# Optimization experiments

Hardware: AMD Instinct MI355X
Metric: run time of the kernel (lower is better)

The kernel has to match this reference:

```python
import jax, jax.numpy as jnp
import numpy as np
from jax import lax

HEADS, DHEAD, LMARK, PINV_ITERS = 8, 64, 256, 6
LN_EPS = 1e-5
DIM_IN, DIM_HID, N_CLASSES, N_INST = 1024, 512, 2, 16384


def layer_norm(x, g, b):
    mu = x.mean(-1, keepdims=True)
    var = ((x - mu) ** 2).mean(-1, keepdims=True)
    return (x - mu) * lax.rsqrt(var + LN_EPS) * g + b


def pinv_iter(x):
    # Newton-Schulz Moore-Penrose iteration (lucidrains nystrom-attention)
    ax = jnp.abs(x)
    z = jnp.swapaxes(x, -1, -2) / (ax.sum(-1).max() * ax.sum(-2).max())
    I = jnp.eye(x.shape[-1], dtype=x.dtype)
    for _ in range(PINV_ITERS):
        xz = x @ z
        z = 0.25 * z @ (13.0 * I - xz @ (15.0 * I - xz @ (7.0 * I - xz)))
    return z


def nystrom_attention(x, qkv_w, out_w, out_b, res_w):
    b, n, _ = x.shape
    pad = (-n) % LMARK  # pad at FRONT so n divisible by num_landmarks
    xp = jnp.pad(x, ((0, 0), (pad, 0), (0, 0)))
    npad = n + pad
    qkv = xp @ qkv_w.T  # (b, npad, 3*h*d)
    q, k, v = jnp.split(qkv, 3, axis=-1)
    sh = lambda t: t.reshape(b, npad, HEADS, DHEAD).transpose(0, 2, 1, 3)  # bhnd
    q, k, v = sh(q), sh(k), sh(v)
    q = q * (DHEAD ** -0.5)
    l = npad // LMARK  # tokens per landmark
    lm = lambda t: t.reshape(b, HEADS, LMARK, l, DHEAD).mean(3)
    ql, kl = lm(q), lm(k)
    a1 = jax.nn.softmax(jnp.einsum('bhid,bhjd->bhij', q, kl), -1)   # (b,h,npad,m)
    a2 = jax.nn.softmax(jnp.einsum('bhid,bhjd->bhij', ql, kl), -1)  # (b,h,m,m)
    a3 = jax.nn.softmax(jnp.einsum('bhid,bhjd->bhij', ql, k), -1)   # (b,h,m,npad)
    out = (a1 @ pinv_iter(a2)) @ (a3 @ v)
    # depthwise residual conv over sequence dim per head: kernel (33,1)
    res = lax.conv_general_dilated(v, res_w, (1, 1), [(16, 16), (0, 0)],
                                   dimension_numbers=('NCHW', 'OIHW', 'NCHW'),
                                   feature_group_count=HEADS)
    out = out + res
    out = out.transpose(0, 2, 1, 3).reshape(b, npad, HEADS * DHEAD)
    out = out @ out_w.T + out_b
    return out[:, -n:]


def depthwise(x, w, b, k):
    y = lax.conv_general_dilated(x, w, (1, 1), [(k // 2, k // 2)] * 2,
                                 dimension_numbers=('NCHW', 'OIHW', 'NCHW'),
                                 feature_group_count=x.shape[1])
    return y + b[None, :, None, None]


def ppeg(x, w7, b7, w5, b5, w3, b3):
    B, n1, C = x.shape
    cls_t, feat = x[:, :1], x[:, 1:]
    H = int(round(float(np.sqrt(n1 - 1))))
    f = feat.transpose(0, 2, 1).reshape(B, C, H, H)
    f = f + depthwise(f, w7, b7, 7) + depthwise(f, w5, b5, 5) + depthwise(f, w3, b3, 3)
    f = f.reshape(B, C, H * H).transpose(0, 2, 1)
    return jnp.concatenate([cls_t, f], axis=1)


def setup_inputs() -> dict:
    key = jax.random.key(0)
    ks = jax.random.split(key, 32)
    s = 0.02
    inner = HEADS * DHEAD
    d = {
        'X': jax.random.normal(ks[0], (1, N_INST, DIM_IN), jnp.float32),
        'fc1_w': jax.random.normal(ks[1], (DIM_HID, DIM_IN)) * s,
        'fc1_b': jnp.zeros((DIM_HID,)),
        'cls_token': jax.random.normal(ks[2], (1, 1, DIM_HID)),
        'ln1_g': jnp.ones((DIM_HID,)), 'ln1_b': jnp.zeros((DIM_HID,)),
        'qkv1_w': jax.random.normal(ks[3], (3 * inner, DIM_HID)) * s,
        'out1_w': jax.random.normal(ks[4], (DIM_HID, inner)) * s,
        'out1_b': jnp.zeros((DIM_HID,)),
        'res1_w': jax.random.normal(ks[5], (HEADS, 1, 33, 1)) * s,
        'w7': jax.random.normal(ks[6], (DIM_HID, 1, 7, 7)) * s, 'b7': jnp.zeros((DIM_HID,)),
        'w5': jax.random.normal(ks[7], (DIM_HID, 1, 5, 5)) * s, 'b5': jnp.zeros((DIM_HID,)),
        'w3': jax.random.normal(ks[8], (DIM_HID, 1, 3, 3)) * s, 'b3': jnp.zeros((DIM_HID,)),
        'ln2_g': jnp.ones((DIM_HID,)), 'ln2_b': jnp.zeros((DIM_HID,)),
        'qkv2_w': jax.random.normal(ks[9], (3 * inner, DIM_HID)) * s,
        'out2_w': jax.random.normal(ks[10], (DIM_HID, inner)) * s,
        'out2_b': jnp.zeros((DIM_HID,)),
        'res2_w': jax.random.normal(ks[11], (HEADS, 1, 33, 1)) * s,
        'lnf_g': jnp.ones((DIM_HID,)), 'lnf_b': jnp.zeros((DIM_HID,)),
        'fc2_w': jax.random.normal(ks[12], (N_CLASSES, DIM_HID)) * s,
        'fc2_b': jnp.zeros((N_CLASSES,)),
    }
    return d


def reference(X, fc1_w, fc1_b, cls_token, ln1_g, ln1_b, qkv1_w, out1_w, out1_b, res1_w,
              w7, b7, w5, b5, w3, b3, ln2_g, ln2_b, qkv2_w, out2_w, out2_b, res2_w,
              lnf_g, lnf_b, fc2_w, fc2_b):
    h = jax.nn.relu(X @ fc1_w.T + fc1_b)  # (1, N, dim_hid)
    B, Hn, C = h.shape
    _H = int(np.ceil(np.sqrt(Hn)))
    add_len = _H * _H - Hn
    h = jnp.concatenate([h, h[:, :add_len]], axis=1)  # pad to square by cycling
    h = jnp.concatenate([jnp.broadcast_to(cls_token, (B, 1, C)), h], axis=1)
    h = h + nystrom_attention(layer_norm(h, ln1_g, ln1_b), qkv1_w, out1_w, out1_b, res1_w)
    h = ppeg(h, w7, b7, w5, b5, w3, b3)
    h = h + nystrom_attention(layer_norm(h, ln2_g, ln2_b), qkv2_w, out2_w, out2_b, res2_w)
    h = layer_norm(h, lnf_g, lnf_b)[:, 0]
    return h @ fc2_w.T + fc2_b  # (1, n_classes)
```

## Files before the change

kernel.cpp:

```cpp
#include <hip/hip_runtime.h>
#include <hip/hip_bf16.h>

static const int S    = 16640;
static const int PADR = 255;
static const int NT   = 16385;
static const int CH   = 512;

typedef unsigned short u16;
typedef __attribute__((ext_vector_type(8))) short short8_t;
typedef __attribute__((ext_vector_type(4))) float float4_t;

__device__ __forceinline__ float b2f(u16 x) {
  union { unsigned u; float f; } t; t.u = (unsigned)x << 16; return t.f;
}
__device__ __forceinline__ u16 f2b(float x) {
  union { float f; unsigned u; } t; t.f = x;
  unsigned r = t.u + 0x7fff + ((t.u >> 16) & 1);
  return (u16)(r >> 16);
}

__device__ __forceinline__ void gload_lds16(const u16* g, u16* l) {
  __builtin_amdgcn_global_load_lds(
      (const __attribute__((address_space(1))) unsigned int*)(g),
      (__attribute__((address_space(3))) unsigned int*)(l), 16, 0, 0);
}

__device__ __forceinline__ float warpSum(float v) {
#pragma unroll
  for (int off = 32; off; off >>= 1) v += __shfl_xor(v, off);
  return v;
}
__device__ __forceinline__ float warpMax(float v) {
#pragma unroll
  for (int off = 32; off; off >>= 1) v = fmaxf(v, __shfl_xor(v, off));
  return v;
}
__device__ __forceinline__ float blockSum(float v) {
  __shared__ float sm[8];
  int lane = threadIdx.x & 63, wv = threadIdx.x >> 6;
  v = warpSum(v);
  __syncthreads();
  if (lane == 0) sm[wv] = v;
  __syncthreads();
  float t = 0.f;
  int nw = blockDim.x >> 6;
  for (int i = 0; i < nw; i++) t += sm[i];
  return t;
}
__device__ __forceinline__ float blockMax(float v) {
  __shared__ float sm[8];
  int lane = threadIdx.x & 63, wv = threadIdx.x >> 6;
  v = warpMax(v);
  __syncthreads();
  if (lane == 0) sm[wv] = v;
  __syncthreads();
  float t = -1e30f;
  int nw = blockDim.x >> 6;
  for (int i = 0; i < nw; i++) t = fmaxf(t, sm[i]);
  return t;
}

__global__ __launch_bounds__(256) void cvt_f2b(const float* __restrict__ in,
                                               u16* __restrict__ out, long n) {
  long i = ((long)blockIdx.x * 256 + threadIdx.x) * 4;
  if (i + 3 < n) {
    float4 v = *(const float4*)(in + i);
    out[i] = f2b(v.x); out[i + 1] = f2b(v.y); out[i + 2] = f2b(v.z); out[i + 3] = f2b(v.w);
  } else {
    for (long j = i; j < n; j++) out[j] = f2b(in[j]);
  }
}

__global__ __launch_bounds__(256) void wm_transpose(const float* __restrict__ Wm,
                                                    u16* __restrict__ WmT) {
  int n = blockIdx.x, head = blockIdx.y, k = threadIdx.x;
  WmT[((long)head * 64 + n) * 256 + k] = f2b(Wm[(long)head * 16384 + k * 64 + n]);
}

__global__ __launch_bounds__(256) void mfma_gemm_qkv(
    const u16* __restrict__ A, const u16* __restrict__ B, float alpha,
    u16* __restrict__ q_o, u16* __restrict__ k_o, u16* __restrict__ v_o, long s64)
{
  __shared__ u16 As[128 * 32];
  __shared__ u16 Bs[128 * 32];
  const int tid = threadIdx.x;
  const int nwg = gridDim.x * gridDim.y;
  int lid = blockIdx.y * gridDim.x + blockIdx.x;
  {
    const int qq = nwg >> 3, rr = nwg & 7;
    const int xcd = lid & 7, loc = lid >> 3;
    lid = (xcd < rr ? xcd * (qq + 1) : rr * (qq + 1) + (xcd - rr) * qq) + loc;
  }
  const int m0 = (lid / gridDim.x) * 128, n0 = (lid % gridDim.x) * 128;
  const int wid = tid >> 6, lane = tid & 63;
  const int wr = wid >> 1, wc = wid & 1;
  const int l15 = lane & 15, l16 = lane >> 4;
  const int r_loc = lane >> 2;
  const int cseg  = lane & 3;
  float4_t acc[4][4] = {};

  for (int k0 = 0; k0 < 512; k0 += 32) {
#pragma unroll
    for (int inst = 0; inst < 2; inst++) {
      const int rbase = wid * 32 + inst * 16;
      const int r = rbase + r_loc;
      const int gseg = cseg ^ ((r >> 1) & 3);
      gload_lds16(A + (long)(m0 + r) * 512 + k0 + gseg * 8, &As[rbase * 32]);
      gload_lds16(B + (long)(n0 + r) * 512 + k0 + gseg * 8, &Bs[rbase * 32]);
    }
    __syncthreads();
    short8_t af[4], bfr[4];
#pragma unroll
    for (int i = 0; i < 4; i++) {
      int row = wr * 64 + i * 16 + l15;
      af[i] = *(const short8_t*)&As[row * 32 + (l16 ^ ((row >> 1) & 3)) * 8];
      int rowb = wc * 64 + i * 16 + l15;
      bfr[i] = *(const short8_t*)&Bs[rowb * 32 + (l16 ^ ((rowb >> 1) & 3)) * 8];
    }
#pragma unroll
    for (int i = 0; i < 4; i++)
#pragma unroll
      for (int j = 0; j < 4; j++)
        acc[i][j] = __builtin_amdgcn_mfma_f32_16x16x32_bf16(af[i], bfr[j], acc[i][j], 0, 0, 0);
    __syncthreads();
  }

#pragma unroll
  for (int mi = 0; mi < 4; mi++) {
#pragma unroll
    for (int ni = 0; ni < 4; ni++) {
#pragma unroll
      for (int j = 0; j < 4; j++) {
        int r = m0 + wr * 64 + mi * 16 + (l16 << 2) + j;
        int c = n0 + wc * 64 + ni * 16 + l15;
        int sec = c >> 9, hcol = c & 511;
        int head = hcol >> 6, d = hcol & 63;
        u16* dst = (sec == 0) ? q_o : (sec == 1 ? k_o : v_o);
        float o = (sec == 0) ? acc[mi][ni][j] * alpha : acc[mi][ni][j];
        dst[(long)head * s64 + (long)r * 64 + d] = f2b(o);
      }
    }
  }
}

template <typename TA, int EPI>
__global__ __launch_bounds__(256) void mfma_gemm(
    const TA* __restrict__ A, const u16* __restrict__ B, float* __restrict__ C,
    const float* __restrict__ bias, int M, int N, int K,
    int lda, int ldb, int ldc,
    float alpha, float beta,
    u16* __restrict__ q_o, u16* __restrict__ k_o, u16* __restrict__ v_o, long s64)
{
  __shared__ u16 As[128][36];
  __shared__ u16 Bs[128][36];
  const int tid = threadIdx.x;
  const int nwg = gridDim.x * gridDim.y;
  int lid = blockIdx.y * gridDim.x + blockIdx.x;
  {
    const int qq = nwg >> 3, rr = nwg & 7;
    const int xcd = lid & 7, loc = lid >> 3;
    lid = (xcd < rr ? xcd * (qq + 1) : rr * (qq + 1) + (xcd - rr) * qq) + loc;
  }
  const int m0 = (lid / gridDim.x) * 128, n0 = (lid % gridDim.x) * 128;
  const int wid = tid >> 6, lane = tid & 63;
  const int wr = wid >> 1, wc = wid & 1;
  const int l15 = lane & 15, l16 = lane >> 4;
  const int arow = tid >> 1, aseg = (tid & 1) * 16;
  float4_t acc[4][4] = {};

  for (int k0 = 0; k0 < K; k0 += 32) {
    {
      int gm = m0 + arow;
      u16 tmp[16];
      if (gm < M) {
        const TA* src = A + (long)gm * lda + k0 + aseg;
        if constexpr (sizeof(TA) == 2) {
          *(short8_t*)&tmp[0] = *(const short8_t*)src;
          *(short8_t*)&tmp[8] = *(const short8_t*)(src + 8);
        } else {
#pragma unroll
          for (int i4 = 0; i4 < 4; i4++) {
            float4 f = *(const float4*)((const float*)src + i4 * 4);
            tmp[i4 * 4 + 0] = f2b(f.x); tmp[i4 * 4 + 1] = f2b(f.y);
            tmp[i4 * 4 + 2] = f2b(f.z); tmp[i4 * 4 + 3] = f2b(f.w);
          }
        }
      } else {
#pragma unroll
        for (int i = 0; i < 16; i++) tmp[i] = 0;
      }
      *(short8_t*)&As[arow][aseg]     = *(short8_t*)&tmp[0];
      *(short8_t*)&As[arow][aseg + 8] = *(short8_t*)&tmp[8];
    }
    {
      int gn = n0 + arow;
      short8_t v0 = {}, v1 = {};
      if (gn < N) {
        const u16* src = B + (long)gn * ldb + k0 + aseg;
        v0 = *(const short8_t*)src; v1 = *(const short8_t*)(src + 8);
      }
      *(short8_t*)&Bs[arow][aseg]     = v0;
      *(short8_t*)&Bs[arow][aseg + 8] = v1;
    }
    __syncthreads();
    short8_t af[4], bfr[4];
#pragma unroll
    for (int i = 0; i < 4; i++)
      af[i] = *(const short8_t*)&As[wr * 64 + i * 16 + l15][l16 * 8];
#pragma unroll
    for (int i = 0; i < 4; i++)
      bfr[i] = *(const short8_t*)&Bs[wc * 64 + i * 16 + l15][l16 * 8];
#pragma unroll
    for (int i = 0; i < 4; i++)
#pragma unroll
      for (int j = 0; j < 4; j++)
        acc[i][j] = __builtin_amdgcn_mfma_f32_16x16x32_bf16(af[i], bfr[j], acc[i][j], 0, 0, 0);
    __syncthreads();
  }

#pragma unroll
  for (int mi = 0; mi < 4; mi++) {
#pragma unroll
    for (int ni = 0; ni < 4; ni++) {
#pragma unroll
      for (int j = 0; j < 4; j++) {
        int r = m0 + wr * 64 + mi * 16 + l16 * 4 + j;
        int c = n0 + wc * 64 + ni * 16 + l15;
        if (r >= M || c >= N) continue;
        float v = acc[mi][ni][j];
        if constexpr (EPI == 0) {
          long idx = (long)r * ldc + c;
          float o = alpha * v;
          if (bias) o += bias[c];
          if (beta != 0.f) o += beta * C[idx];
          C[idx] = o;
        } else if constexpr (EPI == 1) {
          long idx = (long)r * ldc + c;
          C[idx] = fmaxf(v + bias[c], 0.f);
        } else {
          int sec = c >> 9, hcol = c & 511;
          int head = hcol >> 6, d = hcol & 63;
          u16* dst = (sec == 0) ? q_o : (sec == 1 ? k_o : v_o);
          float o = (sec == 0) ? v * alpha : v;
          dst[(long)head * s64 + (long)r * 64 + d] = f2b(o);
        }
      }
    }
  }
}

template <int MODE, int PREC>
__global__ __launch_bounds__(256) void pinv_gemm(
    const float* __restrict__ A, const float* __restrict__ B,
    float* __restrict__ C, float* __restrict__ C2, float alpha, float beta)
{
  __shared__ u16 Ah[32][36], Bh[32][36];
  __shared__ u16 Al[PREC ? 32 : 1][36], Bl[PREC ? 32 : 1][36];
  const int tid = threadIdx.x;
  const long zoff = (long)blockIdx.z << 16;
  A += zoff; B += zoff; C += zoff;
  if constexpr (MODE == 3) C2 += zoff;
  const int m0 = blockIdx.y * 32, n0 = blockIdx.x * 32;
  const int wid = tid >> 6, lane = tid & 63;
  const int wr = wid >> 1, wc = wid & 1;
  const int l15 = lane & 15, l16 = lane >> 4;
  const int arow = tid >> 3, acol = (tid & 7) * 4;
  float4_t acc = {};

  for (int k0 = 0; k0 < 256; k0 += 32) {
    {
      float4 va = *(const float4*)(A + (long)(m0 + arow) * 256 + k0 + acol);
      float4 vb = *(const float4*)(B + (long)(k0 + arow) * 256 + n0 + acol);
      float fa[4] = {va.x, va.y, va.z, va.w};
      float fb[4] = {vb.x, vb.y, vb.z, vb.w};
#pragma unroll
      for (int i = 0; i < 4; i++) {
        u16 hi = f2b(fa[i]);
        Ah[arow][acol + i] = hi;
        u16 hj = f2b(fb[i]);
        Bh[acol + i][arow] = hj;
        if constexpr (PREC) {
          Al[arow][acol + i] = f2b(fa[i] - b2f(hi));
          Bl[acol + i][arow] = f2b(fb[i] - b2f(hj));
        }
      }
    }
    __syncthreads();
    short8_t ah = *(const short8_t*)&Ah[wr * 16 + l15][l16 * 8];
    short8_t bh = *(const short8_t*)&Bh[wc * 16 + l15][l16 * 8];
    acc = __builtin_amdgcn_mfma_f32_16x16x32_bf16(ah, bh, acc, 0, 0, 0);
    if constexpr (PREC) {
      short8_t al = *(const short8_t*)&Al[wr * 16 + l15][l16 * 8];
      short8_t bl = *(const short8_t*)&Bl[wc * 16 + l15][l16 * 8];
      acc = __builtin_amdgcn_mfma_f32_16x16x32_bf16(ah, bl, acc, 0, 0, 0);
      acc = __builtin_amdgcn_mfma_f32_16x16x32_bf16(al, bh, acc, 0, 0, 0);
    }
    __syncthreads();
  }

#pragma unroll
  for (int j = 0; j < 4; j++) {
    int r = m0 + wr * 16 + l16 * 4 + j;
    int c = n0 + wc * 16 + l15;
    long idx = (long)r * 256 + c;
    float v = acc[j];
    if constexpr (MODE == 0) {
      C[idx] = alpha * v;
    } else if constexpr (MODE == 3) {
      C[idx] = v;
      C2[idx] = ((r == c) ? beta : 0.f) - v;
    } else {
      C[idx] = ((r == c) ? beta : 0.f) - v;
    }
  }
}

__global__ __launch_bounds__(256) void a2_fused(
    const u16* __restrict__ qlb, const u16* __restrict__ klb,
    float* __restrict__ a2)
{
  __shared__ u16 KW[256 * 72];
  const int tid = threadIdx.x;
  const int w = tid >> 6, lane = tid & 63;
  const int l15 = lane & 15, l16 = lane >> 4;
  const int head = blockIdx.y;
  const int row0 = blockIdx.x * 64 + w * 16;

  const u16* klh = klb + (long)head * 16384;
#pragma unroll
  for (int i = 0; i < 4; i++) {
    int idx = tid + i * 256;
    int row = idx >> 2, seg = (idx & 3) << 4;
    const u16* src = klh + row * 64 + seg;
    *(short8_t*)&KW[row * 72 + seg]     = *(const short8_t*)src;
    *(short8_t*)&KW[row * 72 + seg + 8] = *(const short8_t*)(src + 8);
  }
  short8_t aq[2];
#pragma unroll
  for (int slab = 0; slab < 2; slab++)
    aq[slab] = *(const short8_t*)(qlb + (long)head * 16384 + (long)(row0 + l15) * 64 + slab * 32 + l16 * 8);
  __syncthreads();

  float4_t sacc[16] = {};
#pragma unroll
  for (int nt = 0; nt < 16; nt++)
#pragma unroll
    for (int slab = 0; slab < 2; slab++) {
      short8_t bfr = *(const short8_t*)&KW[(nt * 16 + l15) * 72 + slab * 32 + l16 * 8];
      sacc[nt] = __builtin_amdgcn_mfma_f32_16x16x32_bf16(aq[slab], bfr, sacc[nt], 0, 0, 0);
    }
#pragma unroll
  for (int reg = 0; reg < 4; reg++) {
    float m = -1e30f;
#pragma unroll
    for (int nt = 0; nt < 16; nt++) m = fmaxf(m, sacc[nt][reg]);
#pragma unroll
    for (int mk = 1; mk <= 8; mk <<= 1) m = fmaxf(m, __shfl_xor(m, mk));
    float s = 0.f;
#pragma unroll
    for (int nt = 0; nt < 16; nt++) { float e = __expf(sacc[nt][reg] - m); sacc[nt][reg] = e; s += e; }
#pragma unroll
    for (int mk = 1; mk <= 8; mk <<= 1) s += __shfl_xor(s, mk);
    float rcp = 1.f / s;
#pragma unroll
    for (int nt = 0; nt < 16; nt++)
      a2[(long)head * 65536 + (long)(row0 + 4 * l16 + reg) * 256 + nt * 16 + l15] =
          sacc[nt][reg] * rcp;
  }
}

__global__ __launch_bounds__(256) void attn_a1(
    const u16* __restrict__ qb, const u16* __restrict__ klb,
    const u16* __restrict__ WmT, float* __restrict__ F, long s64)
{
  __shared__ u16 KW[256 * 72];
  __shared__ u16 Ps[64 * 136];
  const int tid = threadIdx.x;
  const int w = tid >> 6, lane = tid & 63;
  const int l15 = lane & 15, l16 = lane >> 4;
  const int head = blockIdx.y;
  const int row0 = blockIdx.x * 64 + w * 16;

  const u16* klh = klb + (long)head * 16384;
#pragma unroll
  for (int i = 0; i < 4; i++) {
    int idx = tid + i * 256;
    int row = idx >> 2, seg = (idx & 3) << 4;
    const u16* src = klh + row * 64 + seg;
    *(short8_t*)&KW[row * 72 + seg]     = *(const short8_t*)src;
    *(short8_t*)&KW[row * 72 + seg + 8] = *(const short8_t*)(src + 8);
  }
  short8_t aq[2];
#pragma unroll
  for (int slab = 0; slab < 2; slab++)
    aq[slab] = *(const short8_t*)(qb + (long)head * s64 + (long)(row0 + l15) * 64 + slab * 32 + l16 * 8);
  __syncthreads();

  float4_t sacc[16] = {};
#pragma unroll
  for (int nt = 0; nt < 16; nt++)
#pragma unroll
    for (int slab = 0; slab < 2; slab++) {
      short8_t bfr = *(const short8_t*)&KW[(nt * 16 + l15) * 72 + slab * 32 + l16 * 8];
      sacc[nt] = __builtin_amdgcn_mfma_f32_16x16x32_bf16(aq[slab], bfr, sacc[nt], 0, 0, 0);
    }
  float rcp[4];
#pragma unroll
  for (int reg = 0; reg < 4; reg++) {
    float m = -1e30f;
#pragma unroll
    for (int nt = 0; nt < 16; nt++) m = fmaxf(m, sacc[nt][reg]);
#pragma unroll
    for (int mk = 1; mk <= 8; mk <<= 1) m = fmaxf(m, __shfl_xor(m, mk));
    float s = 0.f;
#pragma unroll
    for (int nt = 0; nt < 16; nt++) { float e = __expf(sacc[nt][reg] - m); sacc[nt][reg] = e; s += e; }
#pragma unroll
    for (int mk = 1; mk <= 8; mk <<= 1) s += __shfl_xor(s, mk);
    rcp[reg] = 1.f / s;
  }
  __syncthreads();

  const u16* wmh = WmT + (long)head * 16384;
#pragma unroll
  for (int i = 0; i < 4; i++) {
    int idx = tid + i * 256;
    int row = idx >> 4, seg = (idx & 15) << 4;
    const u16* src = wmh + row * 256 + seg;
    *(short8_t*)&KW[row * 264 + seg]     = *(const short8_t*)src;
    *(short8_t*)&KW[row * 264 + seg + 8] = *(const short8_t*)(src + 8);
  }
#pragma unroll
  for (int nt = 0; nt < 8; nt++)
#pragma unroll
    for (int reg = 0; reg < 4; reg++)
      Ps[(w * 16 + 4 * l16 + reg) * 136 + nt * 16 + l15] = f2b(sacc[nt][reg]);
  __syncthreads();

  float4_t oacc[4] = {};
#pragma unroll
  for (int ks = 0; ks < 4; ks++) {
    short8_t pa = *(const short8_t*)&Ps[(w * 16 + l15) * 136 + ks * 32 + l16 * 8];
#pragma unroll
    for (int vt = 0; vt < 4; vt++) {
      short8_t bv = *(const short8_t*)&KW[(vt * 16 + l15) * 264 + ks * 32 + l16 * 8];
      oacc[vt] = __builtin_amdgcn_mfma_f32_16x16x32_bf16(pa, bv, oacc[vt], 0, 0, 0);
    }
  }
#pragma unroll
  for (int nt = 8; nt < 16; nt++)
#pragma unroll
    for (int reg = 0; reg < 4; reg++)
      Ps[(w * 16 + 4 * l16 + reg) * 136 + (nt - 8) * 16 + l15] = f2b(sacc[nt][reg]);
#pragma unroll
  for (int ks = 4; ks < 8; ks++) {
    short8_t pa = *(const short8_t*)&Ps[(w * 16 + l15) * 136 + (ks - 4) * 32 + l16 * 8];
#pragma unroll
    for (int vt = 0; vt < 4; vt++) {
      short8_t bv = *(const short8_t*)&KW[(vt * 16 + l15) * 264 + ks * 32 + l16 * 8];
      oacc[vt] = __builtin_amdgcn_mfma_f32_16x16x32_bf16(pa, bv, oacc[vt], 0, 0, 0);
    }
  }
#pragma unroll
  for (int vt = 0; vt < 4; vt++)
#pragma unroll
    for (int reg = 0; reg < 4; reg++) {
      int r = row0 + 4 * l16 + reg;
      F[(long)r * CH + head * 64 + vt * 16 + l15] = oacc[vt][reg] * rcp[reg];
    }
}

__global__ __launch_bounds__(256) void attn_a3v_split(
    const u16* __restrict__ qlb, const u16* __restrict__ kb,
    const u16* __restrict__ vb,
    float* __restrict__ pm, float* __restrict__ pl, float* __restrict__ poacc,
    long s64)
{
  __shared__ u16 Vt[64][136];
  __shared__ u16 Kt[128 * 72];
  __shared__ u16 Ps[4][16][136];
  const int tid = threadIdx.x;
  const int w = tid >> 6, lane = tid & 63;
  const int l15 = lane & 15, l16 = lane >> 4;
  const int head = blockIdx.y;
  const int split = blockIdx.z;
  const int row0 = blockIdx.x * 64 + w * 16;

  short8_t aq[2];
#pragma unroll
  for (int slab = 0; slab < 2; slab++)
    aq[slab] = *(const short8_t*)(qlb + (long)head * 16384 + (long)(row0 + l15) * 64 + slab * 32 + l16 * 8);

  float m[4], l[4];
  float4_t oacc[4] = {};
#pragma unroll
  for (int r = 0; r < 4; r++) { m[r] = -1e30f; l[r] = 0.f; }

  const u16* kh = kb + (long)head * s64;
  const u16* vh = vb + (long)head * s64;
  const int vrow = tid >> 1, vhalf = (tid & 1) * 32;

  const int kt0 = split * 10;
  for (int kt = kt0; kt < kt0 + 10; kt++) {
    const int j0 = kt * 128;
    __syncthreads();
    {
      const u16* src = vh + (long)(j0 + vrow) * 64 + vhalf;
#pragma unroll
      for (int i = 0; i < 32; i++) Vt[vhalf + i][vrow] = src[i];
    }
#pragma unroll
    for (int i = 0; i < 2; i++) {
      int idx = tid + i * 256;
      int row = idx >> 2, seg = (idx & 3) << 4;
      const u16* src = kh + (long)(j0 + row) * 64 + seg;
      *(short8_t*)&Kt[row * 72 + seg]     = *(const short8_t*)src;
      *(short8_t*)&Kt[row * 72 + seg + 8] = *(const short8_t*)(src + 8);
    }
    __syncthreads();
    float4_t sacc[8] = {};
#pragma unroll
    for (int nt = 0; nt < 8; nt++)
#pragma unroll
      for (int slab = 0; slab < 2; slab++) {
        short8_t bfr = *(const short8_t*)&Kt[(nt * 16 + l15) * 72 + slab * 32 + l16 * 8];
        sacc[nt] = __builtin_amdgcn_mfma_f32_16x16x32_bf16(aq[slab], bfr, sacc[nt], 0, 0, 0);
      }
    float scale[4];
#pragma unroll
    for (int reg = 0; reg < 4; reg++) {
      float tm = -1e30f;
#pragma unroll
      for (int nt = 0; nt < 8; nt++) tm = fmaxf(tm, sacc[nt][reg]);
#pragma unroll
      for (int mk = 1; mk <= 8; mk <<= 1) tm = fmaxf(tm, __shfl_xor(tm, mk));
      float nm = fmaxf(m[reg], tm);
      scale[reg] = __expf(m[reg] - nm);
      m[reg] = nm;
      float ts = 0.f;
#pragma unroll
      for (int nt = 0; nt < 8; nt++) {
        float e = __expf(sacc[nt][reg] - nm);
        sacc[nt][reg] = e; ts += e;
      }
#pragma unroll
      for (int mk = 1; mk <= 8; mk <<= 1) ts += __shfl_xor(ts, mk);
      l[reg] = l[reg] * scale[reg] + ts;
#pragma unroll
      for (int vt = 0; vt < 4; vt++) oacc[vt][reg] *= scale[reg];
    }
#pragma unroll
    for (int nt = 0; nt < 8; nt++)
#pragma unroll
      for (int reg = 0; reg < 4; reg++)
        Ps[w][4 * l16 + reg][nt * 16 + l15] = f2b(sacc[nt][reg]);
#pragma unroll
    for (int ks = 0; ks < 4; ks++) {
      short8_t pa = *(const short8_t*)&Ps[w][l15][ks * 32 + l16 * 8];
#pragma unroll
      for (int vt = 0; vt < 4; vt++) {
        short8_t bv = *(const short8_t*)&Vt[vt * 16 + l15][ks * 32 + l16 * 8];
        oacc[vt] = __builtin_amdgcn_mfma_f32_16x16x32_bf16(pa, bv, oacc[vt], 0, 0, 0);
      }
    }
  }
#pragma unroll
  for (int reg = 0; reg < 4; reg++) {
    int r = row0 + 4 * l16 + reg;
    long pidx = ((long)(head * 13 + split) << 8) + r;
    if (l15 == 0) { pm[pidx] = m[reg]; pl[pidx] = l[reg]; }
#pragma unroll
    for (int vt = 0; vt < 4; vt++)
      poacc[(pidx << 6) + vt * 16 + l15] = oacc[vt][reg];
  }
}

__global__ __launch_bounds__(64) void a3v_merge(const float* __restrict__ pm,
    const float* __restrict__ pl, const float* __restrict__ poacc,
    float* __restrict__ w3v)
{
  int hb = blockIdx.x;
  int head = hb >> 8, row = hb & 255;
  int d = threadIdx.x;
  float M = -1e30f;
  for (int sp = 0; sp < 13; sp++)
    M = fmaxf(M, pm[((long)(head * 13 + sp) << 8) + row]);
  float num = 0.f, den = 0.f;
  for (int sp = 0; sp < 13; sp++) {
    long pidx = ((long)(head * 13 + sp) << 8) + row;
    float sc = __expf(pm[pidx] - M);
    den += pl[pidx] * sc;
    num += poacc[(pidx << 6) + d] * sc;
  }
  w3v[((long)head << 14) + ((long)row << 6) + d] = num / den;
}

template <bool BT, int MODE>
__global__ __launch_bounds__(256) void mm_kernel(
    const float* __restrict__ A, const float* __restrict__ Bm, float* __restrict__ C,
    const float* __restrict__ bias,
    int M, int N, int K, int lda, int ldb, int ldc,
    long sA, long sB, long sC, float alpha, float beta, long s64)
{
  __shared__ float As[16][64];
  __shared__ float Bs[16][64];
  const int bz = blockIdx.z;
  A  += (long)bz * sA;
  Bm += (long)bz * sB;
  C  += (long)bz * sC;
  const int m0 = blockIdx.y * 64, n0 = blockIdx.x * 64;
  const int tid = threadIdx.x;
  const int tm = tid >> 4, tn = tid & 15;
  const int ar = tid >> 2;
  const int ac = (tid & 3) << 2;
  float acc[4][4] = {};
  for (int k0 = 0; k0 < K; k0 += 16) {
#pragma unroll
    for (int i = 0; i < 4; i++) {
      int gm = m0 + ar, gk = k0 + ac + i;
      As[ac + i][ar] = (gm < M && gk < K) ? A[(long)gm * lda + gk] : 0.f;
    }
    if constexpr (BT) {
#pragma unroll
      for (int i = 0; i < 4; i++) {
        int gn = n0 + ar, gk = k0 + ac + i;
        Bs[ac + i][ar] = (gn < N && gk < K) ? Bm[(long)gn * ldb + gk] : 0.f;
      }
    } else {
      int bk = tid >> 4;
      int bn = (tid & 15) << 2;
#pragma unroll
      for (int i = 0; i < 4; i++) {
        int gk = k0 + bk, gn = n0 + bn + i;
        Bs[bk][bn + i] = (gk < K && gn < N) ? Bm[(long)gk * ldb + gn] : 0.f;
      }
    }
    __syncthreads();
#pragma unroll
    for (int kk = 0; kk < 16; kk++) {
      float a[4], b[4];
#pragma unroll
      for (int i = 0; i < 4; i++) { a[i] = As[kk][tm * 4 + i]; b[i] = Bs[kk][tn * 4 + i]; }
#pragma unroll
      for (int i = 0; i < 4; i++)
#pragma unroll
        for (int j = 0; j < 4; j++)
          acc[i][j] = fmaf(a[i], b[j], acc[i][j]);
    }
    __syncthreads();
  }
#pragma unroll
  for (int i = 0; i < 4; i++) {
    int row = m0 + tm * 4 + i;
    if (row >= M) continue;
#pragma unroll
    for (int j = 0; j < 4; j++) {
      int col = n0 + tn * 4 + j;
      if (col >= N) continue;
      long idx = (long)row * ldc + col;
      float v = acc[i][j];
      float o = alpha * v;
      if (bias) o += bias[col];
      C[idx] = (beta != 0.f) ? o + beta * C[idx] : o;
    }
  }
}

__global__ void cls_copy(const float* __restrict__ c, float* __restrict__ h) {
  h[threadIdx.x] = c[threadIdx.x];
}

__global__ __launch_bounds__(256) void ln_pad_b(const float* __restrict__ h,
    const float* __restrict__ g, const float* __restrict__ b,
    u16* __restrict__ out, int pad)
{
  int s = blockIdx.x, t = threadIdx.x;
  u16* o = out + (long)s * CH;
  if (s < pad) { o[t] = 0; o[t + 256] = 0; return; }
  const float* x = h + (long)(s - pad) * CH;
  float x0 = x[t], x1 = x[t + 256];
  float mu = blockSum(x0 + x1) * (1.f / 512.f);
  float d0 = x0 - mu, d1 = x1 - mu;
  float var = blockSum(d0 * d0 + d1 * d1) * (1.f / 512.f);
  float rs = rsqrtf(var + 1e-5f);
  o[t]       = f2b(d0 * rs * g[t]       + b[t]);
  o[t + 256] = f2b(d1 * rs * g[t + 256] + b[t + 256]);
}

__global__ __launch_bounds__(64) void landmark_b2(const u16* __restrict__ q,
    const u16* __restrict__ k,
    float* __restrict__ ql, float* __restrict__ kl,
    u16* __restrict__ qlb, u16* __restrict__ klb) {
  int isK = blockIdx.x >> 11;
  int hb = blockIdx.x & 2047;
  int d = threadIdx.x;
  int hh = hb >> 8, j = hb & 255;
  const u16* base = isK ? k : q;
  const u16* src = base + ((long)hh * S + (long)j * 65) * 64 + d;
  float s = 0.f;
  for (int g2 = 0; g2 < 65; g2++) s += b2f(src[(long)g2 * 64]);
  s *= (1.f / 65.f);
  float* outf = isK ? kl : ql;
  u16* outb = isK ? klb : qlb;
  outf[(long)hb * 64 + d] = s;
  outb[(long)hb * 64 + d] = f2b(s);
}

__global__ __launch_bounds__(256) void colabs(const float* __restrict__ a2, float* __restrict__ cs) {
  int hb = blockIdx.x; int hh = hb >> 8, j = hb & 255;
  float s = blockSum(fabsf(a2[((long)hh * 256 + threadIdx.x) * 256 + j]));
  if (threadIdx.x == 0) cs[hb] = s;
}
__global__ __launch_bounds__(256) void scaleinv(const float* __restrict__ cs,
                                                float* __restrict__ inv) {
  float m2 = -1e30f;
  for (int i = threadIdx.x; i < 2048; i += 256) m2 = fmaxf(m2, cs[i]);
  m2 = blockMax(m2);
  if (threadIdx.x == 0) inv[0] = 1.f / m2;
}
__global__ __launch_bounds__(256) void z0k(const float* __restrict__ a2,
                                           const float* __restrict__ inv, float* __restrict__ z) {
  int hb = blockIdx.x; int hh = hb >> 8, i = hb & 255; int j = threadIdx.x;
  z[(long)hb * 256 + j] = a2[((long)hh * 256 + j) * 256 + i] * inv[0];
}

__global__ __launch_bounds__(256) void resconv2(const u16* __restrict__ v,
    const float* __restrict__ w, float* __restrict__ F)
{
  __shared__ u16 T[160][64];
  __shared__ float ws[33];
  const int hh = blockIdx.y;
  const int p0 = blockIdx.x * 128;
  const int tid = threadIdx.x;
  if (tid < 33) ws[tid] = w[hh * 33 + tid];
  const u16* vh = v + (long)hh * S * 64;
  for (int idx = tid; idx < 640; idx += 256) {
    int row = idx >> 2, seg = (idx & 3) * 16;
    int j = p0 - 16 + row;
    short8_t a = {}, b = {};
    if (0 <= j && j < S) {
      const u16* src = vh + (long)j * 64 + seg;
      a = *(const short8_t*)src; b = *(const short8_t*)(src + 8);
    }
    *(short8_t*)&T[row][seg]     = a;
    *(short8_t*)&T[row][seg + 8] = b;
  }
  __syncthreads();
  const int d = tid & 63;
  const int pg = tid >> 6;
  float wreg[33];
#pragma unroll
  for (int t = 0; t < 33; t++) wreg[t] = ws[t];
#pragma unroll
  for (int g = 0; g < 4; g++) {
    const int base = pg * 32 + g * 8;
    float win[40];
#pragma unroll
    for (int i = 0; i < 40; i++) win[i] = b2f(T[base + i][d]);
#pragma unroll
    for (int p = 0; p < 8; p++) {
      float acc = 0.f;
#pragma unroll
      for (int t = 0; t < 33; t++) acc = fmaf(wreg[t], win[p + t], acc);
      F[(long)(p0 + base + p) * CH + hh * 64 + d] += acc;
    }
  }
}

__global__ __launch_bounds__(256) void transpose_feat(const float* __restrict__ h, float* __restrict__ f) {
  __shared__ float tile[32][33];
  int p0 = blockIdx.x * 32;
  int c0 = blockIdx.y * 32;
  int tx = threadIdx.x & 31, ty = threadIdx.x >> 5;
  for (int i = 0; i < 32; i += 8)
    tile[ty + i][tx] = h[(long)(1 + p0 + ty + i) * CH + c0 + tx];
  __syncthreads();
  for (int i = 0; i < 32; i += 8)
    f[(long)(c0 + ty + i) * 16384 + p0 + tx] = tile[tx][ty + i];
}

__global__ __launch_bounds__(256) void ppeg_tile(const float* __restrict__ f,
    const float* __restrict__ w7, const float* __restrict__ b7,
    const float* __restrict__ w5, const float* __restrict__ b5,
    const float* __restrict__ w3, const float* __restrict__ b3,
    float* __restrict__ fo)
{
  __shared__ float T[38][40];
  __shared__ float W7s[49], W5s[25], W3s[9];
  int c = blockIdx.y;
  int ty0 = (blockIdx.x >> 2) * 32, tx0 = (blockIdx.x & 3) * 32;
  int tid = threadIdx.x;
  if (tid < 49) W7s[tid] = w7[c * 49 + tid];
  if (tid < 25) W5s[tid] = w5[c * 25 + tid];
  if (tid < 9)  W3s[tid] = w3[c * 9 + tid];
  const float* fc = f + (long)c * 16384;
  for (int idx = tid; idx < 38 * 38; idx += 256) {
    int r = idx / 38, cc = idx - r * 38;
    int y = ty0 + r - 3, x = tx0 + cc - 3;
    T[r][cc] = (0 <= y && y < 128 && 0 <= x && x < 128) ? fc[y * 128 + x] : 0.f;
  }
  __syncthreads();
  const int x = tid & 31, y0 = (tid >> 5) * 4;
  float bsum = b7[c] + b5[c] + b3[c];
  float acc[4];
#pragma unroll
  for (int p = 0; p < 4; p++) acc[p] = T[y0 + p + 3][x + 3] + bsum;
#pragma unroll
  for (int dx = 0; dx < 7; dx++) {
    float col[10];
#pragma unroll
    for (int r = 0; r < 10; r++) col[r] = T[y0 + r][x + dx];
#pragma unroll
    for (int dy = 0; dy < 7; dy++) {
      float wv = W7s[dy * 7 + dx];
#pragma unroll
      for (int p = 0; p < 4; p++) acc[p] = fmaf(wv, col[p + dy], acc[p]);
    }
  }
#pragma unroll
  for (int dx = 0; dx < 5; dx++) {
    float col[8];
#pragma unroll
    for (int r = 0; r < 8; r++) col[r] = T[y0 + 1 + r][x + dx + 1];
#pragma unroll
    for (int dy = 0; dy < 5; dy++) {
      float wv = W5s[dy * 5 + dx];
#pragma unroll
      for (int p = 0; p < 4; p++) acc[p] = fmaf(wv, col[p + dy], acc[p]);
    }
  }
#pragma unroll
  for (int dx = 0; dx < 3; dx++) {
    float col[6];
#pragma unroll
    for (int r = 0; r < 6; r++) col[r] = T[y0 + 2 + r][x + dx + 2];
#pragma unroll
    for (int dy = 0; dy < 3; dy++) {
      float wv = W3s[dy * 3 + dx];
#pragma unroll
      for (int p = 0; p < 4; p++) acc[p] = fmaf(wv, col[p + dy], acc[p]);
    }
  }
#pragma unroll
  for (int p = 0; p < 4; p++)
    fo[(long)c * 16384 + (ty0 + y0 + p) * 128 + tx0 + x] = acc[p];
}

__global__ __launch_bounds__(256) void transpose_back(const float* __restrict__ fo, float* __restrict__ h) {
  __shared__ float tile[32][33];
  int p0 = blockIdx.x * 32;
  int c0 = blockIdx.y * 32;
  int tx = threadIdx.x & 31, ty = threadIdx.x >> 5;
  for (int i = 0; i < 32; i += 8)
    tile[ty + i][tx] = fo[(long)(c0 + ty + i) * 16384 + p0 + tx];
  __syncthreads();
  for (int i = 0; i < 32; i += 8)
    h[(long)(1 + p0 + ty + i) * CH + c0 + tx] = tile[tx][ty + i];
}

__global__ __launch_bounds__(256) void final_k(const float* __restrict__ h,
    const float* __restrict__ g, const float* __restrict__ b,
    const float* __restrict__ w, const float* __restrict__ fb, float* __restrict__ out)
{
  int t = threadIdx.x;
  float x0 = h[t], x1 = h[t + 256];
  float mu = blockSum(x0 + x1) * (1.f / 512.f);
  float d0 = x0 - mu, d1 = x1 - mu;
  float var = blockSum(d0 * d0 + d1 * d1) * (1.f / 512.f);
  float rs = rsqrtf(var + 1e-5f);
  float y0 = d0 * rs * g[t]       + b[t];
  float y1 = d1 * rs * g[t + 256] + b[t + 256];
  float s0 = blockSum(y0 * w[t]       + y1 * w[t + 256]);
  float s1 = blockSum(y0 * w[512 + t] + y1 * w[512 + t + 256]);
  if (t == 0) {
    out[0] = s0 + fb[0];
    out[1] = s1 + fb[1];
  }
}

struct AttnW {
  const float *lng, *lnb, *qkvw, *outw, *outb, *resw;
};

static void run_attn(const AttnW& Wt, const u16* qkvw_b, const u16* outw_b,
                     float* h, u16* hn_b, u16* qb, u16* kb, u16* vb, float* F,
                     float* ql, float* kl, u16* qlb, u16* klb,
                     float* w3v, float* Wm, u16* WmT_b,
                     float* a2, float* xz, float* t1, float* t2, float* zA, float* zB,
                     float* cs, float* inv,
                     float* pm, float* pl, float* poacc,
                     hipStream_t stream)
{
  const long s64 = (long)S * 64;
  ln_pad_b<<<S, 256, 0, stream>>>(h, Wt.lng, Wt.lnb, hn_b, PADR);
  mfma_gemm_qkv<<<dim3(12, 130, 1), 256, 0, stream>>>(
      hn_b, qkvw_b, 0.125f, qb, kb, vb, s64);
  landmark_b2<<<4096, 64, 0, stream>>>(qb, kb, ql, kl, qlb, klb);
  a2_fused<<<dim3(4, 8), 256, 0, stream>>>(qlb, klb, a2);
  colabs<<<2048, 256, 0, stream>>>(a2, cs);
  scaleinv<<<1, 256, 0, stream>>>(cs, inv);
  z0k<<<2048, 256, 0, stream>>>(a2, inv, zA);
  float* zc = zA; float* zo = zB;
  for (int it = 0; it < 5; it++) {
    pinv_gemm<3, 0><<<dim3(8, 8, 8), 256, 0, stream>>>(a2, zc, xz, t1, 1.f, 7.f);
    pinv_gemm<4, 0><<<dim3(8, 8, 8), 256, 0, stream>>>(xz, t1, t2, nullptr, 1.f, 15.f);
    pinv_gemm<4, 0><<<dim3(8, 8, 8), 256, 0, stream>>>(xz, t2, t1, nullptr, 1.f, 13.f);
    pinv_gemm<0, 0><<<dim3(8, 8, 8), 256, 0, stream>>>(zc, t1, zo, nullptr, 0.25f, 0.f);
    float* tmp = zc; zc = zo; zo = tmp;
  }
  pinv_gemm<3, 1><<<dim3(8, 8, 8), 256, 0, stream>>>(a2, zc, xz, t1, 1.f, 7.f);
  pinv_gemm<4, 1><<<dim3(8, 8, 8), 256, 0, stream>>>(xz, t1, t2, nullptr, 1.f, 15.f);
  pinv_gemm<4, 1><<<dim3(8, 8, 8), 256, 0, stream>>>(xz, t2, t1, nullptr, 1.f, 13.f);
  pinv_gemm<0, 1><<<dim3(8, 8, 8), 256, 0, stream>>>(zc, t1, zo, nullptr, 0.25f, 0.f);
  { float* tmp = zc; zc = zo; zo = tmp; }
  attn_a3v_split<<<dim3(4, 8, 13), 256, 0, stream>>>(qlb, kb, vb, pm, pl, poacc, s64);
  a3v_merge<<<2048, 64, 0, stream>>>(pm, pl, poacc, w3v);
  mm_kernel<false, 0><<<dim3(1, 4, 8), 256, 0, stream>>>(
      zc, w3v, Wm, nullptr, 256, 64, 256, 256, 64, 64, 65536, 16384, 16384, 1.f, 0.f, 0);
  wm_transpose<<<dim3(64, 8, 1), 256, 0, stream>>>(Wm, WmT_b);
  attn_a1<<<dim3(260, 8, 1), 256, 0, stream>>>(qb, klb, WmT_b, F, s64);
  resconv2<<<dim3(130, 8, 1), 256, 0, stream>>>(vb, Wt.resw, F);
  mfma_gemm<float, 0><<<dim3(4, 129, 1), 256, 0, stream>>>(
      F + (long)PADR * CH, outw_b, h, Wt.outb, NT, 512, 512, 512, 512, 512,
      1.f, 1.f, nullptr, nullptr, nullptr, 0);
}

extern "C" void kernel_launch(void* const* d_in, const int* in_sizes, int n_in,
                              void* d_out, int out_size, void* d_ws, size_t ws_size,
                              hipStream_t stream)
{
  const float* X      = (const float*)d_in[0];
  const float* fc1w   = (const float*)d_in[1];
  const float* fc1b   = (const float*)d_in[2];
  const float* clstok = (const float*)d_in[3];
  AttnW w1{ (const float*)d_in[4], (const float*)d_in[5], (const float*)d_in[6],
            (const float*)d_in[7], (const float*)d_in[8], (const float*)d_in[9] };
  const float* w7 = (const float*)d_in[10]; const float* b7 = (const float*)d_in[11];
  const float* w5 = (const float*)d_in[12]; const float* b5 = (const float*)d_in[13];
  const float* w3 = (const float*)d_in[14]; const float* b3 = (const float*)d_in[15];
  AttnW w2{ (const float*)d_in[16], (const float*)d_in[17], (const float*)d_in[18],
            (const float*)d_in[19], (const float*)d_in[20], (const float*)d_in[21] };
  const float* lnfg = (const float*)d_in[22];
  const float* lnfb = (const float*)d_in[23];
  const float* fc2w = (const float*)d_in[24];
  const float* fc2b = (const float*)d_in[25];
  float* out = (float*)d_out;

  char* wsb = (char*)d_ws;
  size_t off = 0;
  auto alloc = [&](size_t nbytes) {
    void* p = wsb + off;
    off = (off + nbytes + 255) & ~(size_t)255;
    return p;
  };
  float* h    = (float*)alloc((size_t)NT * CH * 4);
  float* F    = (float*)alloc((size_t)S * CH * 4);
  u16*  hn_b  = (u16*)alloc((size_t)S * CH * 2);
  u16*  qb    = (u16*)alloc((size_t)S * CH * 2);
  u16*  kb    = (u16*)alloc((size_t)S * CH * 2);
  u16*  vb    = (u16*)alloc((size_t)S * CH * 2);
  char* big   = (char*)alloc(33554432);
  u16*  fc1w_b = (u16*)alloc(524288 * 2);
  u16*  qkv1_b = (u16*)alloc(786432 * 2);
  u16*  qkv2_b = (u16*)alloc(786432 * 2);
  u16*  out1_b = (u16*)alloc(262144 * 2);
  u16*  out2_b = (u16*)alloc(262144 * 2);
  float* ql   = (float*)alloc(131072 * 4);
  float* kl   = (float*)alloc(131072 * 4);
  u16*  qlb   = (u16*)alloc(131072 * 2);
  u16*  klb   = (u16*)alloc(131072 * 2);
  float* w3v  = (float*)alloc(131072 * 4);
  float* Wm   = (float*)alloc(131072 * 4);
  u16*  WmT_b = (u16*)alloc(131072 * 2);
  float* a2   = (float*)alloc(524288 * 4);
  float* xz   = (float*)alloc(524288 * 4);
  float* t1   = (float*)alloc(524288 * 4);
  float* t2   = (float*)alloc(524288 * 4);
  float* zA   = (float*)alloc(524288 * 4);
  float* zB   = (float*)alloc(524288 * 4);
  float* cs   = (float*)alloc(2048 * 4);
  float* inv  = (float*)alloc(256);
  float* pm   = (float*)alloc((size_t)8 * 13 * 256 * 4);
  float* pl   = (float*)alloc((size_t)8 * 13 * 256 * 4);
  float* poacc = (float*)alloc((size_t)8 * 13 * 256 * 64 * 4);
  (void)in_sizes; (void)n_in; (void)out_size; (void)ws_size;

  cvt_f2b<<<512, 256, 0, stream>>>(fc1w, fc1w_b, 524288);
  cvt_f2b<<<768, 256, 0, stream>>>(w1.qkvw, qkv1_b, 786432);
  cvt_f2b<<<768, 256, 0, stream>>>(w2.qkvw, qkv2_b, 786432);
  cvt_f2b<<<256, 256, 0, stream>>>(w1.outw, out1_b, 262144);
  cvt_f2b<<<256, 256, 0, stream>>>(w2.outw, out2_b, 262144);

  cls_copy<<<1, 512, 0, stream>>>(clstok, h);
  mfma_gemm<float, 1><<<dim3(4, 128, 1), 256, 0, stream>>>(
      X, fc1w_b, h + CH, fc1b, 16384, 512, 1024, 1024, 1024, 512,
      1.f, 0.f, nullptr, nullptr, nullptr, 0);

  run_attn(w1, qkv1_b, out1_b, h, hn_b, qb, kb, vb, F, ql, kl, qlb, klb,
           w3v, Wm, WmT_b, a2, xz, t1, t2, zA, zB, cs, inv,
           pm, pl, poacc, stream);

  float* fppeg = (float*)big;
  transpose_feat<<<dim3(512, 16, 1), 256, 0, stream>>>(h, fppeg);
  ppeg_tile<<<dim3(16, 512, 1), 256, 0, stream>>>(fppeg, w7, b7, w5, b5, w3, b3, F);
  transpose_back<<<dim3(512, 16, 1), 256, 0, stream>>>(F, h);

  run_attn(w2, qkv2_b, out2_b, h, hn_b, qb, kb, vb, F, ql, kl, qlb, klb,
           w3v, Wm, WmT_b, a2, xz, t1, t2, zA, zB, cs, inv,
           pm, pl, poacc, stream);

  final_k<<<1, 256, 0, stream>>>(h, lnfg, lnfb, fc2w, fc2b, out);
}
```

Measured before the change: 1.083 ms.

## Unify GEMMs on LDS-direct bf16 kernel, store attention output in bf16

Replaces the generic register-staged GEMM with a templated version of the global_load_lds swizzled QKV kernel, used for fc1, QKV and the out-projection. The fp32 input X is converted once to bf16 so fc1 can use the direct-to-LDS path. The attention output buffer F becomes bf16, written by attn_a1 and updated by resconv2, which halves its traffic and lets the out-projection read bf16. This adds a full conversion pass over X and drops bounds checks on loads, so the final M tile of the out-projection reads past NT rows; the Fb buffer is padded to cover that. The residual is also rounded to bf16 before being added.

```diff
diff --git a/kernel.cpp b/kernel.cpp
--- a/kernel.cpp
+++ b/kernel.cpp
@@ -77,8 +77,11 @@
   WmT[((long)head * 64 + n) * 256 + k] = f2b(Wm[(long)head * 16384 + k * 64 + n]);
 }
 
-__global__ __launch_bounds__(256) void mfma_gemm_qkv(
-    const u16* __restrict__ A, const u16* __restrict__ B, float alpha,
+template <int EPI>
+__global__ __launch_bounds__(256) void mfma_gemm_g(
+    const u16* __restrict__ A, const u16* __restrict__ B, float* __restrict__ C,
+    const float* __restrict__ bias, int M, int N, int K,
+    int lda, int ldb, int ldc, float alpha, float beta,
     u16* __restrict__ q_o, u16* __restrict__ k_o, u16* __restrict__ v_o, long s64)
 {
   __shared__ u16 As[128 * 32];
@@ -99,14 +102,14 @@
   const int cseg  = lane & 3;
   float4_t acc[4][4] = {};
 
-  for (int k0 = 0; k0 < 512; k0 += 32) {
+  for (int k0 = 0; k0 < K; k0 += 32) {
 #pragma unroll
     for (int inst = 0; inst < 2; inst++) {
       const int rbase = wid * 32 + inst * 16;
       const int r = rbase + r_loc;
       const int gseg = cseg ^ ((r >> 1) & 3);
-      gload_lds16(A + (long)(m0 + r) * 512 + k0 + gseg * 8, &As[rbase * 32]);
-      gload_lds16(B + (long)(n0 + r) * 512 + k0 + gseg * 8, &Bs[rbase * 32]);
+      gload_lds16(A + (long)(m0 + r) * lda + k0 + gseg * 8, &As[rbase * 32]);
+      gload_lds16(B + (long)(n0 + r) * ldb + k0 + gseg * 8, &Bs[rbase * 32]);
     }
     __syncthreads();
     short8_t af[4], bfr[4];
@@ -132,99 +135,6 @@
 #pragma unroll
       for (int j = 0; j < 4; j++) {
         int r = m0 + wr * 64 + mi * 16 + (l16 << 2) + j;
-        int c = n0 + wc * 64 + ni * 16 + l15;
-        int sec = c >> 9, hcol = c & 511;
-        int head = hcol >> 6, d = hcol & 63;
-        u16* dst = (sec == 0) ? q_o : (sec == 1 ? k_o : v_o);
-        float o = (sec == 0) ? acc[mi][ni][j] * alpha : acc[mi][ni][j];
-        dst[(long)head * s64 + (long)r * 64 + d] = f2b(o);
-      }
-    }
-  }
-}
-
-template <typename TA, int EPI>
-__global__ __launch_bounds__(256) void mfma_gemm(
-    const TA* __restrict__ A, const u16* __restrict__ B, float* __restrict__ C,
-    const float* __restrict__ bias, int M, int N, int K,
-    int lda, int ldb, int ldc,
-    float alpha, float beta,
-    u16* __restrict__ q_o, u16* __restrict__ k_o, u16* __restrict__ v_o, long s64)
-{
-  __shared__ u16 As[128][36];
-  __shared__ u16 Bs[128][36];
-  const int tid = threadIdx.x;
-  const int nwg = gridDim.x * gridDim.y;
-  int lid = blockIdx.y * gridDim.x + blockIdx.x;
-  {
-    const int qq = nwg >> 3, rr = nwg & 7;
-    const int xcd = lid & 7, loc = lid >> 3;
-    lid = (xcd < rr ? xcd * (qq + 1) : rr * (qq + 1) + (xcd - rr) * qq) + loc;
-  }
-  const int m0 = (lid / gridDim.x) * 128, n0 = (lid % gridDim.x) * 128;
-  const int wid = tid >> 6, lane = tid & 63;
-  const int wr = wid >> 1, wc = wid & 1;
-  const int l15 = lane & 15, l16 = lane >> 4;
-  const int arow = tid >> 1, aseg = (tid & 1) * 16;
-  float4_t acc[4][4] = {};
-
-  for (int k0 = 0; k0 < K; k0 += 32) {
-    {
-      int gm = m0 + arow;
-      u16 tmp[16];
-      if (gm < M) {
-        const TA* src = A + (long)gm * lda + k0 + aseg;
-        if constexpr (sizeof(TA) == 2) {
-          *(short8_t*)&tmp[0] = *(const short8_t*)src;
-          *(short8_t*)&tmp[8] = *(const short8_t*)(src + 8);
-        } else {
-#pragma unroll
-          for (int i4 = 0; i4 < 4; i4++) {
-            float4 f = *(const float4*)((const float*)src + i4 * 4);
-            tmp[i4 * 4 + 0] = f2b(f.x); tmp[i4 * 4 + 1] = f2b(f.y);
-            tmp[i4 * 4 + 2] = f2b(f.z); tmp[i4 * 4 + 3] = f2b(f.w);
-          }
-        }
-      } else {
-#pragma unroll
-        for (int i = 0; i < 16; i++) tmp[i] = 0;
-      }
-      *(short8_t*)&As[arow][aseg]     = *(short8_t*)&tmp[0];
-      *(short8_t*)&As[arow][aseg + 8] = *(short8_t*)&tmp[8];
-    }
-    {
-      int gn = n0 + arow;
-      short8_t v0 = {}, v1 = {};
-      if (gn < N) {
-        const u16* src = B + (long)gn * ldb + k0 + aseg;
-        v0 = *(const short8_t*)src; v1 = *(const short8_t*)(src + 8);
-      }
-      *(short8_t*)&Bs[arow][aseg]     = v0;
-      *(short8_t*)&Bs[arow][aseg + 8] = v1;
-    }
-    __syncthreads();
-    short8_t af[4], bfr[4];
-#pragma unroll
-    for (int i = 0; i < 4; i++)
-      af[i] = *(const short8_t*)&As[wr * 64 + i * 16 + l15][l16 * 8];
-#pragma unroll
-    for (int i = 0; i < 4; i++)
-      bfr[i] = *(const short8_t*)&Bs[wc * 64 + i * 16 + l15][l16 * 8];
-#pragma unroll
-    for (int i = 0; i < 4; i++)
-#pragma unroll
-      for (int j = 0; j < 4; j++)
-        acc[i][j] = __builtin_amdgcn_mfma_f32_16x16x32_bf16(af[i], bfr[j], acc[i][j], 0, 0, 0);
-    __syncthreads();
-  }
-
-#pragma unroll
-  for (int mi = 0; mi < 4; mi++) {
-#pragma unroll
-    for (int ni = 0; ni < 4; ni++) {
-#pragma unroll
-      for (int j = 0; j < 4; j++) {
-        int r = m0 + wr * 64 + mi * 16 + l16 * 4 + j;
         int c = n0 + wc * 64 + ni * 16 + l15;
         if (r >= M || c >= N) continue;
         float v = acc[mi][ni][j];
@@ -371,7 +281,7 @@
 
 __global__ __launch_bounds__(256) void attn_a1(
     const u16* __restrict__ qb, const u16* __restrict__ klb,
-    const u16* __restrict__ WmT, float* __restrict__ F, long s64)
+    const u16* __restrict__ WmT, u16* __restrict__ Fb, long s64)
 {
   __shared__ u16 KW[256 * 72];
   __shared__ u16 Ps[64 * 136];
@@ -466,7 +376,7 @@
 #pragma unroll
     for (int reg = 0; reg < 4; reg++) {
       int r = row0 + 4 * l16 + reg;
-      F[(long)r * CH + head * 64 + vt * 16 + l15] = oacc[vt][reg] * rcp[reg];
+      Fb[(long)r * CH + head * 64 + vt * 16 + l15] = f2b(oacc[vt][reg] * rcp[reg]);
     }
 }
 
@@ -725,7 +635,7 @@
 }
 
 __global__ __launch_bounds__(256) void resconv2(const u16* __restrict__ v,
-    const float* __restrict__ w, float* __restrict__ F)
+    const float* __restrict__ w, u16* __restrict__ Fb)
 {
   __shared__ u16 T[160][64];
   __shared__ float ws[33];
@@ -762,7 +672,8 @@
       float acc = 0.f;
 #pragma unroll
       for (int t = 0; t < 33; t++) acc = fmaf(wreg[t], win[p + t], acc);
-      F[(long)(p0 + base + p) * CH + hh * 64 + d] += acc;
+      long idx = (long)(p0 + base + p) * CH + hh * 64 + d;
+      Fb[idx] = f2b(b2f(Fb[idx]) + acc);
     }
   }
 }
@@ -883,7 +794,7 @@
 };
 
 static void run_attn(const AttnW& Wt, const u16* qkvw_b, const u16* outw_b,
-                     float* h, u16* hn_b, u16* qb, u16* kb, u16* vb, float* F,
+                     float* h, u16* hn_b, u16* qb, u16* kb, u16* vb, u16* Fb,
                      float* ql, float* kl, u16* qlb, u16* klb,
                      float* w3v, float* Wm, u16* WmT_b,
                      float* a2, float* xz, float* t1, float* t2, float* zA, float* zB,
@@ -893,8 +804,9 @@
 {
   const long s64 = (long)S * 64;
   ln_pad_b<<<S, 256, 0, stream>>>(h, Wt.lng, Wt.lnb, hn_b, PADR);
-  mfma_gemm_qkv<<<dim3(12, 130, 1), 256, 0, stream>>>(
-      hn_b, qkvw_b, 0.125f, qb, kb, vb, s64);
+  mfma_gemm_g<2><<<dim3(12, 130, 1), 256, 0, stream>>>(
+      hn_b, qkvw_b, nullptr, nullptr, S, 1536, 512, 512, 512, 0,
+      0.125f, 0.f, qb, kb, vb, s64);
   landmark_b2<<<4096, 64, 0, stream>>>(qb, kb, ql, kl, qlb, klb);
   a2_fused<<<dim3(4, 8), 256, 0, stream>>>(qlb, klb, a2);
   colabs<<<2048, 256, 0, stream>>>(a2, cs);
@@ -918,10 +830,10 @@
   mm_kernel<false, 0><<<dim3(1, 4, 8), 256, 0, stream>>>(
       zc, w3v, Wm, nullptr, 256, 64, 256, 256, 64, 64, 65536, 16384, 16384, 1.f, 0.f, 0);
   wm_transpose<<<dim3(64, 8, 1), 256, 0, stream>>>(Wm, WmT_b);
-  attn_a1<<<dim3(260, 8, 1), 256, 0, stream>>>(qb, klb, WmT_b, F, s64);
-  resconv2<<<dim3(130, 8, 1), 256, 0, stream>>>(vb, Wt.resw, F);
-  mfma_gemm<float, 0><<<dim3(4, 129, 1), 256, 0, stream>>>(
-      F + (long)PADR * CH, outw_b, h, Wt.outb, NT, 512, 512, 512, 512, 512,
+  attn_a1<<<dim3(260, 8, 1), 256, 0, stream>>>(qb, klb, WmT_b, Fb, s64);
+  resconv2<<<dim3(130, 8, 1), 256, 0, stream>>>(vb, Wt.resw, Fb);
+  mfma_gemm_g<0><<<dim3(4, 129, 1), 256, 0, stream>>>(
+      Fb + (long)PADR * CH, outw_b, h, Wt.outb, NT, 512, 512, 512, 512, 512,
       1.f, 1.f, nullptr, nullptr, nullptr, 0);
 }
 
@@ -955,6 +867,7 @@
   };
   float* h    = (float*)alloc((size_t)NT * CH * 4);
   float* F    = (float*)alloc((size_t)S * CH * 4);
+  u16*  Fb    = (u16*)alloc((size_t)(S + 256) * CH * 2);
   u16*  hn_b  = (u16*)alloc((size_t)S * CH * 2);
   u16*  qb    = (u16*)alloc((size_t)S * CH * 2);
   u16*  kb    = (u16*)alloc((size_t)S * CH * 2);
@@ -990,13 +903,15 @@
   cvt_f2b<<<768, 256, 0, stream>>>(w2.qkvw, qkv2_b, 786432);
   cvt_f2b<<<256, 256, 0, stream>>>(w1.outw, out1_b, 262144);
   cvt_f2b<<<256, 256, 0, stream>>>(w2.outw, out2_b, 262144);
+  u16* Xb = (u16*)big;
+  cvt_f2b<<<16384, 256, 0, stream>>>(X, Xb, (long)16384 * 1024);
 
   cls_copy<<<1, 512, 0, stream>>>(clstok, h);
-  mfma_gemm<float, 1><<<dim3(4, 128, 1), 256, 0, stream>>>(
-      X, fc1w_b, h + CH, fc1b, 16384, 512, 1024, 1024, 1024, 512,
+  mfma_gemm_g<1><<<dim3(4, 128, 1), 256, 0, stream>>>(
+      Xb, fc1w_b, h + CH, fc1b, 16384, 512, 1024, 1024, 1024, 512,
       1.f, 0.f, nullptr, nullptr, nullptr, 0);
 
-  run_attn(w1, qkv1_b, out1_b, h, hn_b, qb, kb, vb, F, ql, kl, qlb, klb,
+  run_attn(w1, qkv1_b, out1_b, h, hn_b, qb, kb, vb, Fb, ql, kl, qlb, klb,
            w3v, Wm, WmT_b, a2, xz, t1, t2, zA, zB, cs, inv,
            pm, pl, poacc, stream);
 
@@ -1005,7 +920,7 @@
   ppeg_tile<<<dim3(16, 512, 1), 256, 0, stream>>>(fppeg, w7, b7, w5, b5, w3, b3, F);
   transpose_back<<<dim3(512, 16, 1), 256, 0, stream>>>(F, h);
 
-  run_attn(w2, qkv2_b, out2_b, h, hn_b, qb, kb, vb, F, ql, kl, qlb, klb,
+  run_attn(w2, qkv2_b, out2_b, h, hn_b, qb, kb, vb, Fb, ql, kl, qlb, klb,
            w3v, Wm, WmT_b, a2, xz, t1, t2, zA, zB, cs, inv,
            pm, pl, poacc, stream);
 
```

Measured after the change: 1.087 ms. About the same (+0.4%).
